# Kernel optimization log

Measured on AMD Instinct MI355X. Metric: run time of the kernel, lower is better.

The kernel has to match this reference:

```python
import jax, jax.numpy as jnp
import numpy as np

B, T, V = 8, 2048, 4096
BEAM = 8      # beam_size
BLANK = 0     # blank_id=0 in CTCBeamDecoder
TMP = 1.0     # temperature self.tmp


def setup_inputs() -> dict:
    key = jax.random.key(0)
    k1, k2 = jax.random.split(key)
    logits = jax.random.normal(k1, (B, T, V), dtype=jnp.float32)
    # valid frame counts in [T//2, T]
    lengths = jax.random.randint(k2, (B,), T // 2, T + 1).astype(jnp.int32)
    return {"logits": logits, "lengths": lengths}


def _beam_search_single(logP, length):
    """CTC beam search over alignments (no LM) for one utterance.
    logP: [T, V] log-probs, length: scalar valid frame count.
    Returns (collapsed_tokens [T] padded with -1, out_len, best_score).
    """
    scores0, toks0 = jax.lax.top_k(logP[0], BEAM)              # [BEAM]
    toks0 = toks0.astype(jnp.int32)
    bp0 = jnp.zeros((BEAM,), jnp.int32)

    def step(scores, xs):
        t, logp_t = xs
        cand = scores[:, None] + logp_t[None, :]               # [BEAM, V]
        new_scores, flat_idx = jax.lax.top_k(cand.reshape(-1), BEAM)
        bp = (flat_idx // V).astype(jnp.int32)
        tok = (flat_idx % V).astype(jnp.int32)
        valid = t < length
        new_scores = jnp.where(valid, new_scores, scores)
        bp = jnp.where(valid, bp, jnp.arange(BEAM, dtype=jnp.int32))
        tok = jnp.where(valid, tok, jnp.full((BEAM,), BLANK, jnp.int32))
        return new_scores, (tok, bp)

    ts = jnp.arange(1, T)
    final_scores, (toks, bps) = jax.lax.scan(step, scores0, (ts, logP[1:]))
    toks = jnp.concatenate([toks0[None], toks], axis=0)        # [T, BEAM]
    bps = jnp.concatenate([bp0[None], bps], axis=0)            # [T, BEAM]

    # backtrace best beam (index 0 after final top_k)
    def back(beam, xs):
        tok_t, bp_t = xs
        return bp_t[beam], tok_t[beam]
    _, path = jax.lax.scan(back, jnp.int32(0), (toks, bps), reverse=True)  # [T] in time order

    # CTC collapse: drop blanks and consecutive repeats, restrict to valid frames
    tpos = jnp.arange(T)
    prev = jnp.concatenate([jnp.array([-1], jnp.int32), path[:-1]])
    keep = (path != BLANK) & (path != prev) & (tpos < length)
    out_len = keep.sum().astype(jnp.int32)
    pos = jnp.cumsum(keep) - 1                                  # target slot for kept tokens
    idx = jnp.where(keep, pos, T)                               # dump non-kept into slot T
    out = jnp.full((T + 1,), -1, jnp.int32).at[idx].set(jnp.where(keep, path, -1))
    return out[:T], out_len, final_scores[0]


def reference(logits, lengths):
    # logits/tmp then log_softmax (the tensorized part of the torch module)
    logP = jax.nn.log_softmax(logits / TMP, axis=-1)            # [B, T, V]
    tokens, out_lens, best_scores = jax.vmap(_beam_search_single)(logP, lengths)
    return tokens, out_lens, best_scores, logP
```

## Files before the change

### kernel.cpp

```cpp
#include <hip/hip_runtime.h>
#include <cmath>

#define NB 8
#define NT 2048
#define NV 4096
#define NK 12

__device__ __forceinline__ void lds_fence() {
  asm volatile("s_waitcnt lgkmcnt(0)" ::: "memory");
}

__global__ __launch_bounds__(64, 6) void lsm_top12_kernel(
    const float* __restrict__ logits,
    float* __restrict__ out_logP,
    float* __restrict__ topPf,
    int* __restrict__ topI)
{
  const int row  = blockIdx.x;
  const int lane = threadIdx.x;
  const float4* __restrict__ x4 = (const float4*)(logits + (size_t)row * NV);

  float m = -INFINITY;
  float a0 = 0.0f, a1 = 0.0f, a2 = 0.0f, a3 = 0.0f;
  float4 f0 = x4[lane], f1 = x4[lane + 64], f2 = x4[lane + 128],
         f3 = x4[lane + 192];
  #pragma unroll
  for (int c = 0; c < 4; ++c) {
    float4 g0, g1, g2, g3;
    if (c < 3) {
      const int kb = lane + ((c + 1) << 8);
      g0 = x4[kb]; g1 = x4[kb + 64]; g2 = x4[kb + 128]; g3 = x4[kb + 192];
    } else { g0 = f0; g1 = f1; g2 = f2; g3 = f3; }
    float cm = fmaxf(fmaxf(fmaxf(f0.x, f0.y), fmaxf(f0.z, f0.w)),
                     fmaxf(fmaxf(f1.x, f1.y), fmaxf(f1.z, f1.w)));
    cm = fmaxf(cm, fmaxf(fmaxf(fmaxf(f2.x, f2.y), fmaxf(f2.z, f2.w)),
                         fmaxf(fmaxf(f3.x, f3.y), fmaxf(f3.z, f3.w))));
    const float nm = fmaxf(m, cm);
    const float sc = __expf(m - nm);
    a0 = a0 * sc + (__expf(f0.x - nm) + __expf(f1.x - nm) +
                    __expf(f2.x - nm) + __expf(f3.x - nm));
    a1 = a1 * sc + (__expf(f0.y - nm) + __expf(f1.y - nm) +
                    __expf(f2.y - nm) + __expf(f3.y - nm));
    a2 = a2 * sc + (__expf(f0.z - nm) + __expf(f1.z - nm) +
                    __expf(f2.z - nm) + __expf(f3.z - nm));
    a3 = a3 * sc + (__expf(f0.w - nm) + __expf(f1.w - nm) +
                    __expf(f2.w - nm) + __expf(f3.w - nm));
    m = nm;
    f0 = g0; f1 = g1; f2 = g2; f3 = g3;
  }

  float M = m;
  #pragma unroll
  for (int off = 32; off > 0; off >>= 1) M = fmaxf(M, __shfl_xor(M, off, 64));
  float accf = ((a0 + a1) + (a2 + a3)) * __expf(m - M);
  #pragma unroll
  for (int off = 32; off > 0; off >>= 1) accf += __shfl_xor(accf, off, 64);
  const float L32 = logf(accf);

  float lv[NK]; int li[NK];
  #pragma unroll
  for (int z = 0; z < NK; ++z) { lv[z] = -INFINITY; li[z] = 0x7FFFFFFF; }

#define INS(VAL, IDX)                                                       \
  do {                                                                      \
    float _v = (VAL); int _i = (IDX);                                       \
    if (_v > lv[NK - 1]) {                                                  \
      lv[NK - 1] = _v; li[NK - 1] = _i;                                     \
      for (int z = NK - 1; z > 0; --z)                                      \
        if (lv[z] > lv[z - 1]) {                                            \
          float tv = lv[z]; lv[z] = lv[z - 1]; lv[z - 1] = tv;              \
          int   ti = li[z]; li[z] = li[z - 1]; li[z - 1] = ti;              \
        }                                                                   \
    }                                                                       \
  } while (0)

#define DO4(F, KK)                                                          \
  do {                                                                      \
    const int idx = lane + ((KK) << 6);                                     \
    const int vb  = idx << 2;                                               \
    float4 o;                                                               \
    o.x = (F.x - M) - L32;                                                  \
    o.y = (F.y - M) - L32;                                                  \
    o.z = (F.z - M) - L32;                                                  \
    o.w = (F.w - M) - L32;                                                  \
    orow4[idx] = o;                                                         \
    const float g4 = fmaxf(fmaxf(o.x, o.y), fmaxf(o.z, o.w));               \
    if (g4 > lv[NK - 1]) {         \
      INS(o.x, vb); INS(o.y, vb + 1); INS(o.z, vb + 2); INS(o.w, vb + 3);   \
    }                                                                       \
  } while (0)

  float4* __restrict__ orow4 = (float4*)(out_logP + (size_t)row * NV);
  f0 = x4[lane]; f1 = x4[lane + 64]; f2 = x4[lane + 128]; f3 = x4[lane + 192];
  #pragma unroll
  for (int c = 0; c < 4; ++c) {
    float4 g0, g1, g2, g3;
    if (c < 3) {
      const int kb = lane + ((c + 1) << 8);
      g0 = x4[kb]; g1 = x4[kb + 64]; g2 = x4[kb + 128]; g3 = x4[kb + 192];
    } else { g0 = f0; g1 = f1; g2 = f2; g3 = f3; }
    DO4(f0, c * 4 + 0); DO4(f1, c * 4 + 1);
    DO4(f2, c * 4 + 2); DO4(f3, c * 4 + 3);
    f0 = g0; f1 = g1; f2 = g2; f3 = g3;
  }
#undef DO4
#undef INS

  float mv = 0.0f; int mi = 0;
  #pragma unroll
  for (int rr = 0; rr < NK; ++rr) {
    float cv = lv[0]; int ci = li[0];
    #pragma unroll
    for (int off = 32; off > 0; off >>= 1) {
      float ov = __shfl_xor(cv, off, 64);
      int   oi = __shfl_xor(ci, off, 64);
      if (ov > cv || (ov == cv && oi < ci)) { cv = ov; ci = oi; }
    }
    if (rr == 0)    { mv = cv; mi = ci; }
    if (lane == rr) { mv = cv; mi = ci; }
    if (lv[0] == cv && li[0] == ci) {
      for (int z = 0; z < NK - 1; ++z) { lv[z] = lv[z + 1]; li[z] = li[z + 1]; }
      lv[NK - 1] = -INFINITY; li[NK - 1] = 0x7FFFFFFF;
    }
  }
  if (lane < NK) {
    topPf[(size_t)row * NK + lane] = mv;
    topI [(size_t)row * NK + lane] = mi;
  }
}


#define LOADROW(P, V, R)                                                      \
  do {                                                                        \
    const int _r = (R) < NT ? (R) : (NT - 1);                                 \
    P = Pb[(size_t)_r * NK + j_l];                                            \
    V = Ib[(size_t)_r * NK + j_l];                                            \
  } while (0)

#define CMP4(BASE, A0, A1, A2, A3)                                            \
  do {                                                                        \
    const unsigned int lo0 = (unsigned int)__builtin_amdgcn_readlane((int)klo, (BASE));     \
    const unsigned int hi0 = (unsigned int)__builtin_amdgcn_readlane((int)khi, (BASE));     \
    const unsigned int lo1 = (unsigned int)__builtin_amdgcn_readlane((int)klo, (BASE) + 1); \
    const unsigned int hi1 = (unsigned int)__builtin_amdgcn_readlane((int)khi, (BASE) + 1); \
    const unsigned int lo2 = (unsigned int)__builtin_amdgcn_readlane((int)klo, (BASE) + 2); \
    const unsigned int hi2 = (unsigned int)__builtin_amdgcn_readlane((int)khi, (BASE) + 2); \
    const unsigned int lo3 = (unsigned int)__builtin_amdgcn_readlane((int)klo, (BASE) + 3); \
    const unsigned int hi3 = (unsigned int)__builtin_amdgcn_readlane((int)khi, (BASE) + 3); \
    A0 += ((((unsigned long long)hi0 << 32) | lo0) > key) ? 1 : 0;            \
    A1 += ((((unsigned long long)hi1 << 32) | lo1) > key) ? 1 : 0;            \
    A2 += ((((unsigned long long)hi2 << 32) | lo2) > key) ? 1 : 0;            \
    A3 += ((((unsigned long long)hi3 << 32) | lo3) > key) ? 1 : 0;            \
  } while (0)

#define STEP(T, PV, VV)                                                       \
  do {                                                                        \
    const float cand = s + (PV);              \
    const unsigned int cb = ~__float_as_uint(cand);                           \
    const unsigned int flat = (unsigned int)((i_l << 12) | (VV));             \
    const unsigned long long key =                                            \
        ((unsigned long long)cb << 15) | (unsigned long long)(0x7FFFu ^ flat);\
    const unsigned int klo = (unsigned int)key;                               \
    const unsigned int khi = (unsigned int)(key >> 32);                       \
    int r0_ = 0, r1_ = 0, r2_ = 0, r3_ = 0;                                   \
    CMP4(0,  r0_, r1_, r2_, r3_);                                             \
    CMP4(4,  r0_, r1_, r2_, r3_);                                             \
    CMP4(8,  r0_, r1_, r2_, r3_);                                             \
    CMP4(12, r0_, r1_, r2_, r3_);                                             \
    CMP4(16, r0_, r1_, r2_, r3_);                                             \
    CMP4(20, r0_, r1_, r2_, r3_);                                             \
    CMP4(24, r0_, r1_, r2_, r3_);                                             \
    {                                                                         \
      const unsigned int lo0 = (unsigned int)__builtin_amdgcn_readlane((int)klo, 28); \
      const unsigned int hi0 = (unsigned int)__builtin_amdgcn_readlane((int)khi, 28); \
      const unsigned int lo1 = (unsigned int)__builtin_amdgcn_readlane((int)klo, 29); \
      const unsigned int hi1 = (unsigned int)__builtin_amdgcn_readlane((int)khi, 29); \
      const unsigned int lo2 = (unsigned int)__builtin_amdgcn_readlane((int)klo, 30); \
      const unsigned int hi2 = (unsigned int)__builtin_amdgcn_readlane((int)khi, 30); \
      r0_ += ((((unsigned long long)hi0 << 32) | lo0) > key) ? 1 : 0;         \
      r1_ += ((((unsigned long long)hi1 << 32) | lo1) > key) ? 1 : 0;         \
      r2_ += ((((unsigned long long)hi2 << 32) | lo2) > key) ? 1 : 0;         \
    }                                                                         \
    const int rank = (r0_ + r1_) + (r2_ + r3_);                               \
    const bool win = active && (rank < 8);                                    \
    const int sloti = win ? ((T) * 8 + rank) : (NT * 8 + lane);               \
    tokbp[sloti] = (unsigned short)(((VV) << 3) | i_l);                       \
    const int dst4 = win ? (rank << 2) : park4;                               \
    const int pushed =                                                        \
        __builtin_amdgcn_ds_permute(dst4, __float_as_int(cand));              \
    const float w0 = __uint_as_float((unsigned)__builtin_amdgcn_readlane(pushed, 0)); \
    const float w1 = __uint_as_float((unsigned)__builtin_amdgcn_readlane(pushed, 1)); \
    const float w2 = __uint_as_float((unsigned)__builtin_amdgcn_readlane(pushed, 2)); \
    const float w3 = __uint_as_float((unsigned)__builtin_amdgcn_readlane(pushed, 3)); \
    const float w4 = __uint_as_float((unsigned)__builtin_amdgcn_readlane(pushed, 4)); \
    const float w5 = __uint_as_float((unsigned)__builtin_amdgcn_readlane(pushed, 5)); \
    const float w6 = __uint_as_float((unsigned)__builtin_amdgcn_readlane(pushed, 6)); \
    const float w7 = __uint_as_float((unsigned)__builtin_amdgcn_readlane(pushed, 7)); \
    const float sA_ = b0 ? w1 : w0;                                           \
    const float sB_ = b0 ? w3 : w2;                                           \
    const float sC_ = b0 ? w5 : w4;                                           \
    const float sD_ = b0 ? w7 : w6;                                           \
    const float sE_ = b1 ? sB_ : sA_;                                         \
    const float sF_ = b1 ? sD_ : sC_;                                         \
    s = b2 ? sF_ : sE_;                                                       \
  } while (0)

__global__ __launch_bounds__(64) void beam_kernel(
    const float* __restrict__ topPf,
    const int* __restrict__ topI,
    const int* __restrict__ lengths,
    float* __restrict__ out_tok,
    float* __restrict__ out_lenA,
    float* __restrict__ out_scr)
{
  const int b    = blockIdx.x;
  const int lane = threadIdx.x;

  __shared__ unsigned short tokbp[NT * 8 + 64];
  __shared__ unsigned short pathA[NT];

  int len = lengths[b];
  if (len < 1) len = 1;
  if (len > NT) len = NT;

  int i_l = 0, j_l = 0; bool active = false;
  {
    int c = 0;
    #pragma unroll
    for (int i = 0; i < 8; ++i) {
      const int cnt = 12 / (i + 1);
      if (lane >= c && lane < c + cnt) { i_l = i; j_l = lane - c; active = true; }
      c += cnt;
    }
  }
  const bool b0 = (i_l & 1) != 0;
  const bool b1 = (i_l & 2) != 0;
  const bool b2 = (i_l & 4) != 0;
  const int  park4 = (32 + (lane & 31)) << 2;

  const float* __restrict__ Pb = topPf + (size_t)b * NT * NK;
  const int*   __restrict__ Ib = topI  + (size_t)b * NT * NK;

  float s = Pb[i_l];
  if (lane < 8) tokbp[lane] = (unsigned short)(Ib[lane] << 3);

  float pA0, pA1, pA2, pA3, pB0, pB1, pB2, pB3;
  int   vA0, vA1, vA2, vA3, vB0, vB1, vB2, vB3;
  LOADROW(pA0, vA0, 1); LOADROW(pA1, vA1, 2);
  LOADROW(pA2, vA2, 3); LOADROW(pA3, vA3, 4);
  LOADROW(pB0, vB0, 5); LOADROW(pB1, vB1, 6);
  LOADROW(pB2, vB2, 7); LOADROW(pB3, vB3, 8);

  int t = 1;
  for (; t + 7 < len; t += 8) {
    STEP(t,     pA0, vA0);
    STEP(t + 1, pA1, vA1);
    STEP(t + 2, pA2, vA2);
    STEP(t + 3, pA3, vA3);
    LOADROW(pA0, vA0, t + 8);  LOADROW(pA1, vA1, t + 9);
    LOADROW(pA2, vA2, t + 10); LOADROW(pA3, vA3, t + 11);
    STEP(t + 4, pB0, vB0);
    STEP(t + 5, pB1, vB1);
    STEP(t + 6, pB2, vB2);
    STEP(t + 7, pB3, vB3);
    LOADROW(pB0, vB0, t + 12); LOADROW(pB1, vB1, t + 13);
    LOADROW(pB2, vB2, t + 14); LOADROW(pB3, vB3, t + 15);
  }
  if (t     < len) STEP(t,     pA0, vA0);
  if (t + 1 < len) STEP(t + 1, pA1, vA1);
  if (t + 2 < len) STEP(t + 2, pA2, vA2);
  if (t + 3 < len) STEP(t + 3, pA3, vA3);
  if (t + 4 < len) STEP(t + 4, pB0, vB0);
  if (t + 5 < len) STEP(t + 5, pB1, vB1);
  if (t + 6 < len) STEP(t + 6, pB2, vB2);

  lds_fence();
  if (lane == 0) {
    const uint4* __restrict__ rows = (const uint4*)tokbp;
#define EXT(R)                                                                \
    do {                                                                      \
      const unsigned long long half = (beam < 4)                              \
          ? (((unsigned long long)(R).y << 32) | (R).x)                       \
          : (((unsigned long long)(R).w << 32) | (R).z);                      \
      const int e = (int)((half >> ((beam & 3) << 4)) & 0xFFFFu);             \
      pathA[bt] = (unsigned short)(e >> 3);                                   \
      beam = e & 7;                                                           \
      --bt;                                                                   \
    } while (0)
    int beam = 0;
    int bt = len - 1;
    uint4 r0 = rows[bt];
    uint4 r1 = rows[bt >= 1 ? bt - 1 : 0];
    uint4 r2 = rows[bt >= 2 ? bt - 2 : 0];
    uint4 r3 = rows[bt >= 3 ? bt - 3 : 0];
    while (bt >= 7) {
      const uint4 n0 = rows[bt - 4], n1 = rows[bt - 5];
      const uint4 n2 = rows[bt - 6], n3 = rows[bt - 7];
      EXT(r0); EXT(r1); EXT(r2); EXT(r3);
      r0 = n0; r1 = n1; r2 = n2; r3 = n3;
    }
    while (bt >= 0) { const uint4 rr = rows[bt]; EXT(rr); }
#undef EXT
  }
  lds_fence();

  const int CH = NT / 64;
  const int base = lane * CH;
  int cnt = 0;
  for (int k = 0; k < CH; ++k) {
    int tt = base + k;
    if (tt < len) {
      int pt = pathA[tt];
      int pv = (tt > 0) ? (int)pathA[tt - 1] : -1;
      cnt += ((pt != 0) && (pt != pv)) ? 1 : 0;
    }
  }
  int incl = cnt;
  #pragma unroll
  for (int off = 1; off < 64; off <<= 1) {
    int n = __shfl_up(incl, off, 64);
    if (lane >= off) incl += n;
  }
  const int excl  = incl - cnt;
  const int total = __shfl(incl, 63, 64);

  float* __restrict__ ob = out_tok + (size_t)b * NT;
  int pos = excl;
  for (int k = 0; k < CH; ++k) {
    int tt = base + k;
    if (tt < len) {
      int pt = pathA[tt];
      int pv = (tt > 0) ? (int)pathA[tt - 1] : -1;
      if ((pt != 0) && (pt != pv)) { ob[pos] = (float)pt; ++pos; }
    }
  }
  for (int q = total + lane; q < NT; q += 64) ob[q] = -1.0f;

  if (lane == 0) {
    out_lenA[b] = (float)total;
    out_scr[b]  = s;
  }
}

#undef STEP
#undef CMP4
#undef LOADROW

extern "C" void kernel_launch(void* const* d_in, const int* in_sizes, int n_in,
                              void* d_out, int out_size, void* d_ws, size_t ws_size,
                              hipStream_t stream) {
  (void)in_sizes; (void)n_in; (void)out_size; (void)ws_size;
  const float* logits  = (const float*)d_in[0];
  const int*   lengths = (const int*)d_in[1];

  float* out_tok  = (float*)d_out;
  float* out_lenp = out_tok + NB * NT;
  float* out_scr  = out_lenp + NB;
  float* out_logP = out_scr + NB;

  float* topPf = (float*)d_ws;
  int*   topI  = (int*)(topPf + (size_t)NB * NT * NK);

  lsm_top12_kernel<<<NB * NT, 64, 0, stream>>>(logits, out_logP, topPf, topI);
  beam_kernel<<<NB, 64, 0, stream>>>(topPf, topI, lengths, out_tok, out_lenp, out_scr);
}
```

Baseline: 1.461 ms.

## Split softmax/top-12 row across four waves and interleave top-k value/index pairs

The log-softmax plus per-row top-12 kernel now uses 256 threads per row instead of one wave. Each thread holds its four float4s in registers, so the logits are read from global memory once rather than twice. Max and sum are reduced across waves through shared memory, and the four per-wave top-12 lists are merged by wave 0. Top-k scores and indices are stored as interleaved float2 pairs, so the beam kernel fetches both with one load per row. This adds two block barriers and an extra merge pass per row, and leaves each thread with fewer elements for the serial insertion sort.

```diff
diff --git a/kernel.cpp b/kernel.cpp
--- a/kernel.cpp
+++ b/kernel.cpp
@@ -10,52 +10,50 @@
   asm volatile("s_waitcnt lgkmcnt(0)" ::: "memory");
 }
 
-__global__ __launch_bounds__(64, 6) void lsm_top12_kernel(
+__global__ __launch_bounds__(256, 6) void lsm_top12_kernel(
     const float* __restrict__ logits,
     float* __restrict__ out_logP,
-    float* __restrict__ topPf,
-    int* __restrict__ topI)
+    float* __restrict__ topPI)
 {
   const int row  = blockIdx.x;
-  const int lane = threadIdx.x;
+  const int tid  = threadIdx.x;
+  const int lane = tid & 63;
+  const int wid  = tid >> 6;
   const float4* __restrict__ x4 = (const float4*)(logits + (size_t)row * NV);
 
+  __shared__ float smax[4];
+  __shared__ float ssum[4];
+  __shared__ float tv48[48];
+  __shared__ int   ti48[48];
+
+  float4 r[4];
+  #pragma unroll
+  for (int k = 0; k < 4; ++k) r[k] = x4[tid + (k << 8)];
+
   float m = -INFINITY;
+  #pragma unroll
+  for (int k = 0; k < 4; ++k)
+    m = fmaxf(m, fmaxf(fmaxf(r[k].x, r[k].y), fmaxf(r[k].z, r[k].w)));
+  #pragma unroll
+  for (int off = 32; off > 0; off >>= 1) m = fmaxf(m, __shfl_xor(m, off, 64));
+  if (lane == 0) smax[wid] = m;
+  __syncthreads();
+  const float M = fmaxf(fmaxf(smax[0], smax[1]), fmaxf(smax[2], smax[3]));
+
   float a0 = 0.0f, a1 = 0.0f, a2 = 0.0f, a3 = 0.0f;
-  float4 f0 = x4[lane], f1 = x4[lane + 64], f2 = x4[lane + 128],
-         f3 = x4[lane + 192];
-  #pragma unroll
-  for (int c = 0; c < 4; ++c) {
-    float4 g0, g1, g2, g3;
-    if (c < 3) {
-      const int kb = lane + ((c + 1) << 8);
-      g0 = x4[kb]; g1 = x4[kb + 64]; g2 = x4[kb + 128]; g3 = x4[kb + 192];
-    } else { g0 = f0; g1 = f1; g2 = f2; g3 = f3; }
-    float cm = fmaxf(fmaxf(fmaxf(f0.x, f0.y), fmaxf(f0.z, f0.w)),
-                     fmaxf(fmaxf(f1.x, f1.y), fmaxf(f1.z, f1.w)));
-    cm = fmaxf(cm, fmaxf(fmaxf(fmaxf(f2.x, f2.y), fmaxf(f2.z, f2.w)),
-                         fmaxf(fmaxf(f3.x, f3.y), fmaxf(f3.z, f3.w))));
-    const float nm = fmaxf(m, cm);
-    const float sc = __expf(m - nm);
-    a0 = a0 * sc + (__expf(f0.x - nm) + __expf(f1.x - nm) +
-                    __expf(f2.x - nm) + __expf(f3.x - nm));
-    a1 = a1 * sc + (__expf(f0.y - nm) + __expf(f1.y - nm) +
-                    __expf(f2.y - nm) + __expf(f3.y - nm));
-    a2 = a2 * sc + (__expf(f0.z - nm) + __expf(f1.z - nm) +
-                    __expf(f2.z - nm) + __expf(f3.z - nm));
-    a3 = a3 * sc + (__expf(f0.w - nm) + __expf(f1.w - nm) +
-                    __expf(f2.w - nm) + __expf(f3.w - nm));
-    m = nm;
-    f0 = g0; f1 = g1; f2 = g2; f3 = g3;
-  }
-
-  float M = m;
-  #pragma unroll
-  for (int off = 32; off > 0; off >>= 1) M = fmaxf(M, __shfl_xor(M, off, 64));
-  float accf = ((a0 + a1) + (a2 + a3)) * __expf(m - M);
+  #pragma unroll
+  for (int k = 0; k < 4; ++k) {
+    a0 += __expf(r[k].x - M);
+    a1 += __expf(r[k].y - M);
+    a2 += __expf(r[k].z - M);
+    a3 += __expf(r[k].w - M);
+  }
+  float accf = (a0 + a1) + (a2 + a3);
   #pragma unroll
   for (int off = 32; off > 0; off >>= 1) accf += __shfl_xor(accf, off, 64);
-  const float L32 = logf(accf);
+  if (lane == 0) ssum[wid] = accf;
+  __syncthreads();
+  const float L32 = logf((ssum[0] + ssum[1]) + (ssum[2] + ssum[3]));
 
   float lv[NK]; int li[NK];
   #pragma unroll
@@ -74,36 +72,22 @@
     }                                                                       \
   } while (0)
 
-#define DO4(F, KK)                                                          \
-  do {                                                                      \
-    const int idx = lane + ((KK) << 6);                                     \
-    const int vb  = idx << 2;                                               \
-    float4 o;                                                               \
-    o.x = (F.x - M) - L32;                                                  \
-    o.y = (F.y - M) - L32;                                                  \
-    o.z = (F.z - M) - L32;                                                  \
-    o.w = (F.w - M) - L32;                                                  \
-    orow4[idx] = o;                                                         \
-    const float g4 = fmaxf(fmaxf(o.x, o.y), fmaxf(o.z, o.w));               \
-    if (g4 > lv[NK - 1]) {         \
-      INS(o.x, vb); INS(o.y, vb + 1); INS(o.z, vb + 2); INS(o.w, vb + 3);   \
-    }                                                                       \
-  } while (0)
-
   float4* __restrict__ orow4 = (float4*)(out_logP + (size_t)row * NV);
-  f0 = x4[lane]; f1 = x4[lane + 64]; f2 = x4[lane + 128]; f3 = x4[lane + 192];
-  #pragma unroll
-  for (int c = 0; c < 4; ++c) {
-    float4 g0, g1, g2, g3;
-    if (c < 3) {
-      const int kb = lane + ((c + 1) << 8);
-      g0 = x4[kb]; g1 = x4[kb + 64]; g2 = x4[kb + 128]; g3 = x4[kb + 192];
-    } else { g0 = f0; g1 = f1; g2 = f2; g3 = f3; }
-    DO4(f0, c * 4 + 0); DO4(f1, c * 4 + 1);
-    DO4(f2, c * 4 + 2); DO4(f3, c * 4 + 3);
-    f0 = g0; f1 = g1; f2 = g2; f3 = g3;
-  }
-#undef DO4
+  #pragma unroll
+  for (int k = 0; k < 4; ++k) {
+    const int idx = tid + (k << 8);
+    const int vb  = idx << 2;
+    float4 o;
+    o.x = (r[k].x - M) - L32;
+    o.y = (r[k].y - M) - L32;
+    o.z = (r[k].z - M) - L32;
+    o.w = (r[k].w - M) - L32;
+    orow4[idx] = o;
+    const float g4 = fmaxf(fmaxf(o.x, o.y), fmaxf(o.z, o.w));
+    if (g4 > lv[NK - 1]) {
+      INS(o.x, vb); INS(o.y, vb + 1); INS(o.z, vb + 2); INS(o.w, vb + 3);
+    }
+  }
 #undef INS
 
   float mv = 0.0f; int mi = 0;
@@ -123,9 +107,30 @@
       lv[NK - 1] = -INFINITY; li[NK - 1] = 0x7FFFFFFF;
     }
   }
-  if (lane < NK) {
-    topPf[(size_t)row * NK + lane] = mv;
-    topI [(size_t)row * NK + lane] = mi;
+  if (lane < NK) { tv48[wid * NK + lane] = mv; ti48[wid * NK + lane] = mi; }
+  __syncthreads();
+
+  if (wid == 0) {
+    float cv = (lane < 48) ? tv48[lane] : -INFINITY;
+    int   ci = (lane < 48) ? ti48[lane] : 0x7FFFFFFF;
+    float fv = 0.0f; int fi = 0;
+    #pragma unroll
+    for (int rr = 0; rr < NK; ++rr) {
+      float bv = cv; int bi = ci;
+      #pragma unroll
+      for (int off = 32; off > 0; off >>= 1) {
+        float ov = __shfl_xor(bv, off, 64);
+        int   oi = __shfl_xor(bi, off, 64);
+        if (ov > bv || (ov == bv && oi < bi)) { bv = ov; bi = oi; }
+      }
+      if (rr == 0)    { fv = bv; fi = bi; }
+      if (lane == rr) { fv = bv; fi = bi; }
+      if (cv == bv && ci == bi) { cv = -INFINITY; ci = 0x7FFFFFFF; }
+    }
+    if (lane < NK) {
+      float2 pr; pr.x = fv; pr.y = __int_as_float(fi);
+      *(float2*)(topPI + ((size_t)row * NK + lane) * 2) = pr;
+    }
   }
 }
 
@@ -133,8 +138,8 @@
 #define LOADROW(P, V, R)                                                      \
   do {                                                                        \
     const int _r = (R) < NT ? (R) : (NT - 1);                                 \
-    P = Pb[(size_t)_r * NK + j_l];                                            \
-    V = Ib[(size_t)_r * NK + j_l];                                            \
+    const float2 _pr = PIb[(size_t)_r * NK + j_l];                            \
+    P = _pr.x; V = __float_as_int(_pr.y);                                     \
   } while (0)
 
 #define CMP4(BASE, A0, A1, A2, A3)                                            \
@@ -206,8 +211,7 @@
   } while (0)
 
 __global__ __launch_bounds__(64) void beam_kernel(
-    const float* __restrict__ topPf,
-    const int* __restrict__ topI,
+    const float* __restrict__ topPI,
     const int* __restrict__ lengths,
     float* __restrict__ out_tok,
     float* __restrict__ out_lenA,
@@ -238,11 +242,11 @@
   const bool b2 = (i_l & 4) != 0;
   const int  park4 = (32 + (lane & 31)) << 2;
 
-  const float* __restrict__ Pb = topPf + (size_t)b * NT * NK;
-  const int*   __restrict__ Ib = topI  + (size_t)b * NT * NK;
-
-  float s = Pb[i_l];
-  if (lane < 8) tokbp[lane] = (unsigned short)(Ib[lane] << 3);
+  const float2* __restrict__ PIb = (const float2*)topPI + (size_t)b * NT * NK;
+
+  float s = PIb[i_l].x;
+  if (lane < 8)
+    tokbp[lane] = (unsigned short)(__float_as_int(PIb[lane].y) << 3);
 
   float pA0, pA1, pA2, pA3, pB0, pB1, pB2, pB3;
   int   vA0, vA1, vA2, vA3, vB0, vB1, vB2, vB3;
@@ -358,9 +362,8 @@
   float* out_scr  = out_lenp + NB;
   float* out_logP = out_scr + NB;
 
-  float* topPf = (float*)d_ws;
-  int*   topI  = (int*)(topPf + (size_t)NB * NT * NK);
-
-  lsm_top12_kernel<<<NB * NT, 64, 0, stream>>>(logits, out_logP, topPf, topI);
-  beam_kernel<<<NB, 64, 0, stream>>>(topPf, topI, lengths, out_tok, out_lenp, out_scr);
+  float* topPI = (float*)d_ws;
+
+  lsm_top12_kernel<<<NB * NT, 256, 0, stream>>>(logits, out_logP, topPI);
+  beam_kernel<<<NB, 64, 0, stream>>>(topPI, lengths, out_tok, out_lenp, out_scr);
 }
```

Result: slower. 1.548 ms (+5.9%).
